# Performance work log

Hardware: AMD Instinct MI355X
Metric: run time of the kernel (lower is better)

The kernel has to match this reference:

```python
import jax, jax.numpy as jnp
import numpy as np

I, H, O = 64, 512, 64
B, S = 32, 2048


def setup_inputs() -> dict:
    key = jax.random.key(0)
    ks = jax.random.split(key, 8)
    def xavier(k, shape):
        fan_in, fan_out = shape[1], shape[0]
        lim = jnp.sqrt(6.0 / (fan_in + fan_out))
        return jax.random.uniform(k, shape, jnp.float32, -lim, lim)
    return {
        "x": jax.random.normal(ks[0], (B, S, I), jnp.float32),
        "h_0": jnp.zeros((B, H), jnp.float32),
        "Wz": xavier(ks[1], (H, I + H)),
        "Wr": xavier(ks[2], (H, I + H)),
        "Wh": xavier(ks[3], (H, I + H)),
        "bz": jnp.ones((H,), jnp.float32),
        "br": jnp.zeros((H,), jnp.float32),
        "bh": jnp.zeros((H,), jnp.float32),
        "W1": xavier(ks[4], (H, H)),
        "b1": jnp.zeros((H,), jnp.float32),
        "W2": xavier(ks[5], (O, H)),
        "b2": jnp.zeros((O,), jnp.float32),
    }


def reference(x, h_0, Wz, Wr, Wh, bz, br, bh, W1, b1, W2, b2):
    def step(h_prev, x_t):
        combined = jnp.concatenate([x_t, h_prev], axis=1)          # [B, I+H]
        z = jax.nn.sigmoid(combined @ Wz.T + bz)                   # [B, H]
        r = jax.nn.sigmoid(combined @ Wr.T + br)                   # [B, H]
        gate_input = jnp.concatenate([r * h_prev, x_t], axis=1)    # [B, H+I]
        h_hat = jnp.tanh(gate_input @ Wh.T + bh)                   # [B, H]
        h_t = (1.0 - z) * h_prev + z * h_hat
        out = jax.nn.relu(h_t @ W1.T + b1) @ W2.T + b2             # [B, O]
        return h_t, out

    # scan over time: x -> [S, B, I]
    h_last, outs = jax.lax.scan(step, h_0, jnp.swapaxes(x, 0, 1))
    return jnp.swapaxes(outs, 0, 1), h_last  # [B, S, O], [B, H]
```

## Files before the change

kernel.cpp:

```cpp
#include <hip/hip_runtime.h>
#include <stdint.h>

#define S_LEN 2048

typedef unsigned long long u64;
typedef __attribute__((ext_vector_type(8))) short short8;
typedef __attribute__((ext_vector_type(4))) float f32x4;

__device__ __forceinline__ unsigned short f2bf(float f) {
  union { float f; unsigned int u; } v; v.f = f;
  unsigned int u = v.u;
  u = (u + 0x7FFFu + ((u >> 16) & 1u)) >> 16;
  return (unsigned short)u;
}

__device__ __forceinline__ void st_bf(unsigned short* p, unsigned short v) {
  __hip_atomic_store(p, v, __ATOMIC_RELAXED, __HIP_MEMORY_SCOPE_AGENT);
}
__device__ __forceinline__ u64 ld_u64(const unsigned short* p) {
  return __hip_atomic_load((const u64*)p, __ATOMIC_RELAXED, __HIP_MEMORY_SCOPE_AGENT);
}

__global__ void prep_kernel(const float* __restrict__ Wz, const float* __restrict__ Wr,
                            const float* __restrict__ Wh, const float* __restrict__ W1,
                            const float* __restrict__ W2,
                            unsigned short* __restrict__ WgT,
                            unsigned short* __restrict__ W1T,
                            unsigned short* __restrict__ W2T) {
  const int total = 1536 * 576 + 512 * 512 + 64 * 512;
  for (int idx = blockIdx.x * 256 + threadIdx.x; idx < total; idx += gridDim.x * 256) {
    if (idx < 1536 * 576) {
      int row = idx / 576, k = idx % 576;
      float v;
      if (row < 512)       v = Wz[row * 576 + k];
      else if (row < 1024) v = Wr[(row - 512) * 576 + k];
      else {
        int r = row - 1024;
        v = (k < 64) ? Wh[r * 576 + 512 + k] : Wh[r * 576 + (k - 64)];
      }
      WgT[idx] = f2bf(v);
    } else if (idx < 1536 * 576 + 512 * 512) {
      int i = idx - 1536 * 576;
      W1T[i] = f2bf(W1[i]);
    } else {
      int i = idx - 1536 * 576 - 512 * 512;
      W2T[i] = f2bf(W2[i]);
    }
  }
}

__global__ void __launch_bounds__(256, 1) recur_kernel(
    const float* __restrict__ x, const float* __restrict__ h0,
    const float* __restrict__ bz, const float* __restrict__ br,
    const float* __restrict__ bh, const unsigned short* __restrict__ WgT,
    unsigned short* __restrict__ hbuf, unsigned short* __restrict__ rhbuf,
    unsigned short* __restrict__ h_all, float* __restrict__ h_last,
    unsigned int* __restrict__ flags) {
  extern __shared__ char smem[];
  unsigned short* Wf = (unsigned short*)smem;
  unsigned short* Xf = Wf + 6 * 18 * 64 * 8;
  float* hfp = (float*)(Xf + 2 * 64 * 8);

  const int wg = blockIdx.x;
  const int g = wg >> 4, w = wg & 15;
  const int tid = threadIdx.x;
  const int lane = tid & 63, wave = tid >> 6;
  const int crow = (lane >> 4) << 2;
  const int ccol = lane & 15;
  const int ko8 = (lane >> 4) << 3;

  for (int i = tid; i < 6 * 18 * 64; i += 256) {
    int T = i / (18 * 64);
    int kk = (i >> 6) % 18;
    int l = i & 63;
    int row = (T >> 1) * 512 + w * 32 + (T & 1) * 16 + (l & 15);
    int k = kk * 32 + ((l >> 4) << 3);
    uint4 v = *(const uint4*)(WgT + (size_t)row * 576 + k);
    *(uint4*)(Wf + (size_t)i * 8) = v;
  }
  for (int i = tid; i < 512; i += 256) {
    int m = i >> 5, c = i & 31;
    float hv = h0[(size_t)(g * 16 + m) * 512 + w * 32 + c];
    hfp[m * 32 + c] = hv;
    st_bf(hbuf + (size_t)(g * 16 + m) * 512 + w * 32 + c, f2bf(hv));
  }
  const int pm = tid >> 4, pf4 = tid & 15;
  float4 xreg = *(const float4*)(x + ((size_t)(g * 16 + pm) * S_LEN + 0) * 64 + pf4 * 4);
  {
    int c = pf4 >> 1;
    int F = (c >> 2) * 64 + (c & 3) * 16 + pm;
    unsigned short tmp[4] = {f2bf(xreg.x), f2bf(xreg.y), f2bf(xreg.z), f2bf(xreg.w)};
    *(u64*)(Xf + F * 8 + (pf4 & 1) * 4) = *(u64*)tmp;
  }
  __syncthreads();

  unsigned int* myflag = flags + g * 256 + w * 16;
  const unsigned int* gflags = flags + g * 256;
  if (tid == 0)
    __hip_atomic_store(myflag, 1u, __ATOMIC_RELAXED, __HIP_MEMORY_SCOPE_AGENT);

  float bzv = 0.f, brv = 0.f, bhv = 0.f;
  if (wave < 2) { bzv = bz[w * 32 + wave * 16 + ccol]; bhv = bh[w * 32 + wave * 16 + ccol]; }
  else          { brv = br[w * 32 + (wave & 1) * 16 + ccol]; }

  const unsigned short* hsrc  = hbuf  + (size_t)(g * 16 + ccol) * 512 + ko8;
  const unsigned short* rhsrc = rhbuf + (size_t)(g * 16 + ccol) * 512 + ko8;

  float zreg[4];

  for (int t = 0; t < S_LEN; ++t) {
    if (wave == 0) {
      const unsigned int* fl = gflags + (lane & 15) * 16;
      unsigned int it = 0;
      for (;;) {
        unsigned int v = __hip_atomic_load(fl, __ATOMIC_RELAXED, __HIP_MEMORY_SCOPE_AGENT);
        if (__all((int)(v >= (unsigned)(2 * t + 1)))) break;
        if (++it > (1u << 22)) break;
      }
    }
    __syncthreads();

    short8 aarr[16];
#pragma unroll
    for (int kk = 0; kk < 16; ++kk) {
      union { u64 q[2]; short8 v; } u;
      u.q[0] = ld_u64(hsrc + kk * 32);
      u.q[1] = ld_u64(hsrc + kk * 32 + 4);
      aarr[kk] = u.v;
    }
    const unsigned short* Bb = Wf + (size_t)wave * 18 * 512 + lane * 8;
    short8 ax0 = *(const short8*)(Xf + (0 * 64 + lane) * 8);
    short8 ax1 = *(const short8*)(Xf + (1 * 64 + lane) * 8);
    f32x4 acc0 = {0.f, 0.f, 0.f, 0.f}, acc1 = {0.f, 0.f, 0.f, 0.f};
    acc0 = __builtin_amdgcn_mfma_f32_16x16x32_bf16(ax0, *(const short8*)(Bb + 0 * 512), acc0, 0, 0, 0);
    acc1 = __builtin_amdgcn_mfma_f32_16x16x32_bf16(ax1, *(const short8*)(Bb + 1 * 512), acc1, 0, 0, 0);
#pragma unroll
    for (int kk = 0; kk < 16; kk += 2) {
      acc0 = __builtin_amdgcn_mfma_f32_16x16x32_bf16(aarr[kk],     *(const short8*)(Bb + (kk + 2) * 512), acc0, 0, 0, 0);
      acc1 = __builtin_amdgcn_mfma_f32_16x16x32_bf16(aarr[kk + 1], *(const short8*)(Bb + (kk + 3) * 512), acc1, 0, 0, 0);
    }
    f32x4 acc = acc0 + acc1;
    if (wave < 2) {
#pragma unroll
      for (int j = 0; j < 4; ++j)
        zreg[j] = 1.f / (1.f + __expf(-(acc[j] + bzv)));
    } else {
      const int nloc = (wave & 1) * 16 + ccol;
      const int ng = w * 32 + nloc;
#pragma unroll
      for (int j = 0; j < 4; ++j) {
        int m = crow + j;
        float rv = 1.f / (1.f + __expf(-(acc[j] + brv)));
        float rh = rv * hfp[m * 32 + nloc];
        st_bf(rhbuf + (size_t)(g * 16 + m) * 512 + ng, f2bf(rh));
      }
    }
    __syncthreads();
    if (tid == 0)
      __hip_atomic_store(myflag, (unsigned)(2 * t + 2), __ATOMIC_RELAXED, __HIP_MEMORY_SCOPE_AGENT);

    if (wave == 0) {
      const unsigned int* fl = gflags + (lane & 15) * 16;
      unsigned int it = 0;
      for (;;) {
        unsigned int v = __hip_atomic_load(fl, __ATOMIC_RELAXED, __HIP_MEMORY_SCOPE_AGENT);
        if (__all((int)(v >= (unsigned)(2 * t + 2)))) break;
        if (++it > (1u << 22)) break;
      }
    }
    __syncthreads();

    int tn = (t + 1 < S_LEN) ? t + 1 : t;
    xreg = *(const float4*)(x + ((size_t)(g * 16 + pm) * S_LEN + tn) * 64 + pf4 * 4);

    if (wave < 2) {
      short8 barr[16];
#pragma unroll
      for (int kk = 0; kk < 16; ++kk) {
        union { u64 q[2]; short8 v; } u2;
        u2.q[0] = ld_u64(rhsrc + kk * 32);
        u2.q[1] = ld_u64(rhsrc + kk * 32 + 4);
        barr[kk] = u2.v;
      }
      const unsigned short* Bh = Wf + (size_t)(4 + wave) * 18 * 512 + lane * 8;
      f32x4 b0 = {0.f, 0.f, 0.f, 0.f}, b1 = {0.f, 0.f, 0.f, 0.f};
      b0 = __builtin_amdgcn_mfma_f32_16x16x32_bf16(ax0, *(const short8*)(Bh + 0 * 512), b0, 0, 0, 0);
      b1 = __builtin_amdgcn_mfma_f32_16x16x32_bf16(ax1, *(const short8*)(Bh + 1 * 512), b1, 0, 0, 0);
#pragma unroll
      for (int kk = 0; kk < 16; kk += 2) {
        b0 = __builtin_amdgcn_mfma_f32_16x16x32_bf16(barr[kk],     *(const short8*)(Bh + (kk + 2) * 512), b0, 0, 0, 0);
        b1 = __builtin_amdgcn_mfma_f32_16x16x32_bf16(barr[kk + 1], *(const short8*)(Bh + (kk + 3) * 512), b1, 0, 0, 0);
      }
      f32x4 hacc = b0 + b1;
      const int nloc = wave * 16 + ccol;
      const int ng = w * 32 + nloc;
#pragma unroll
      for (int j = 0; j < 4; ++j) {
        int m = crow + j;
        float e = __expf(2.f * (hacc[j] + bhv));
        float hh = 1.f - 2.f / (e + 1.f);
        float hold = hfp[m * 32 + nloc];
        float z = zreg[j];
        float hn = (1.f - z) * hold + z * hh;
        hfp[m * 32 + nloc] = hn;
        unsigned short hb = f2bf(hn);
        st_bf(hbuf + (size_t)(g * 16 + m) * 512 + ng, hb);
        h_all[((size_t)(g * 16 + m) * S_LEN + t) * 512 + ng] = hb;
        if (t == S_LEN - 1) h_last[(size_t)(g * 16 + m) * 512 + ng] = hn;
      }
    }
    __syncthreads();
    if (tid == 0)
      __hip_atomic_store(myflag, (unsigned)(2 * t + 3), __ATOMIC_RELAXED, __HIP_MEMORY_SCOPE_AGENT);

    {
      int c = pf4 >> 1;
      int F = (c >> 2) * 64 + (c & 3) * 16 + pm;
      unsigned short tmp[4] = {f2bf(xreg.x), f2bf(xreg.y), f2bf(xreg.z), f2bf(xreg.w)};
      *(u64*)(Xf + F * 8 + (pf4 & 1) * 4) = *(u64*)tmp;
    }
  }
}

__global__ void __launch_bounds__(256, 1) head_kernel(
    const unsigned short* __restrict__ h_all, const unsigned short* __restrict__ W1T,
    const unsigned short* __restrict__ W2T, const float* __restrict__ b1,
    const float* __restrict__ b2, float* __restrict__ out) {
  extern __shared__ char smem[];
  unsigned short* hs = (unsigned short*)smem;
  unsigned short* act = hs + 64 * 520;

  const int tid = threadIdx.x, lane = tid & 63, wave = tid >> 6;
  const int crow = (lane >> 4) << 2, ccol = lane & 15;
  const size_t row0 = (size_t)blockIdx.x * 64;

  for (int i = tid; i < 64 * 64; i += 256) {
    int r = i >> 6, c8 = i & 63;
    uint4 v = *(const uint4*)(h_all + (row0 + r) * 512 + c8 * 8);
    *(uint4*)(hs + r * 520 + c8 * 8) = v;
  }
  __syncthreads();

  f32x4 acc[8][4];
#pragma unroll
  for (int nt = 0; nt < 8; ++nt)
#pragma unroll
    for (int mt = 0; mt < 4; ++mt) acc[nt][mt] = {0.f, 0.f, 0.f, 0.f};

  for (int k = 0; k < 16; ++k) {
    short8 a[4];
#pragma unroll
    for (int mt = 0; mt < 4; ++mt)
      a[mt] = *(const short8*)(hs + (mt * 16 + ccol) * 520 + k * 32 + ((lane >> 4) << 3));
#pragma unroll
    for (int nt = 0; nt < 8; ++nt) {
      int n0 = (wave * 8 + nt) * 16;
      short8 b = *(const short8*)(W1T + (size_t)(n0 + ccol) * 512 + k * 32 + ((lane >> 4) << 3));
#pragma unroll
      for (int mt = 0; mt < 4; ++mt)
        acc[nt][mt] = __builtin_amdgcn_mfma_f32_16x16x32_bf16(a[mt], b, acc[nt][mt], 0, 0, 0);
    }
  }
#pragma unroll
  for (int nt = 0; nt < 8; ++nt) {
    int n = wave * 128 + nt * 16 + ccol;
    float bias = b1[n];
#pragma unroll
    for (int mt = 0; mt < 4; ++mt)
#pragma unroll
      for (int j = 0; j < 4; ++j) {
        float v = fmaxf(acc[nt][mt][j] + bias, 0.f);
        act[(mt * 16 + crow + j) * 520 + n] = f2bf(v);
      }
  }
  __syncthreads();
  for (int i = tid; i < 64 * 64; i += 256) {
    int r = i >> 6, c8 = i & 63;
    uint4 v = *(const uint4*)(W2T + (size_t)r * 512 + c8 * 8);
    *(uint4*)(hs + r * 520 + c8 * 8) = v;
  }
  __syncthreads();

  f32x4 acc2[4];
#pragma unroll
  for (int nt = 0; nt < 4; ++nt) acc2[nt] = {0.f, 0.f, 0.f, 0.f};
  for (int k = 0; k < 16; ++k) {
    short8 a = *(const short8*)(act + (wave * 16 + ccol) * 520 + k * 32 + ((lane >> 4) << 3));
#pragma unroll
    for (int nt = 0; nt < 4; ++nt) {
      short8 b = *(const short8*)(hs + (nt * 16 + ccol) * 520 + k * 32 + ((lane >> 4) << 3));
      acc2[nt] = __builtin_amdgcn_mfma_f32_16x16x32_bf16(a, b, acc2[nt], 0, 0, 0);
    }
  }
#pragma unroll
  for (int nt = 0; nt < 4; ++nt) {
    int o = nt * 16 + ccol;
    float bias = b2[o];
#pragma unroll
    for (int j = 0; j < 4; ++j) {
      int r = wave * 16 + crow + j;
      out[(row0 + r) * 64 + o] = acc2[nt][j] + bias;
    }
  }
}

extern "C" void kernel_launch(void* const* d_in, const int* in_sizes, int n_in,
                              void* d_out, int out_size, void* d_ws, size_t ws_size,
                              hipStream_t stream) {
  const float* x  = (const float*)d_in[0];
  const float* h0 = (const float*)d_in[1];
  const float* Wz = (const float*)d_in[2];
  const float* Wr = (const float*)d_in[3];
  const float* Wh = (const float*)d_in[4];
  const float* bz = (const float*)d_in[5];
  const float* br = (const float*)d_in[6];
  const float* bh = (const float*)d_in[7];
  const float* W1 = (const float*)d_in[8];
  const float* b1 = (const float*)d_in[9];
  const float* W2 = (const float*)d_in[10];
  const float* b2 = (const float*)d_in[11];

  char* ws = (char*)d_ws;
  size_t off = 0;
  unsigned int*   flags = (unsigned int*)(ws + off);   off += 4096;
  unsigned short* hbuf  = (unsigned short*)(ws + off); off += 32 * 512 * 2;
  unsigned short* rhbuf = (unsigned short*)(ws + off); off += 32 * 512 * 2;
  unsigned short* WgT   = (unsigned short*)(ws + off); off += (size_t)1536 * 576 * 2;
  unsigned short* W1T   = (unsigned short*)(ws + off); off += (size_t)512 * 512 * 2;
  unsigned short* W2T   = (unsigned short*)(ws + off); off += (size_t)64 * 512 * 2;
  unsigned short* h_all = (unsigned short*)(ws + off); off += (size_t)32 * 2048 * 512 * 2;

  float* out = (float*)d_out;
  float* h_last = out + (size_t)32 * 2048 * 64;

  hipMemsetAsync(flags, 0, 4096, stream);
  hipLaunchKernelGGL(prep_kernel, dim3(1024), dim3(256), 0, stream,
                     Wz, Wr, Wh, W1, W2, WgT, W1T, W2T);

  const int recur_lds = (6 * 18 * 64 * 8 + 2 * 64 * 8) * 2 + 16 * 32 * 4;
  hipFuncSetAttribute(reinterpret_cast<const void*>(&recur_kernel),
                      hipFuncAttributeMaxDynamicSharedMemorySize, recur_lds);
  hipLaunchKernelGGL(recur_kernel, dim3(32), dim3(256), recur_lds, stream,
                     x, h0, bz, br, bh, WgT, hbuf, rhbuf, h_all, h_last, flags);

  const int head_lds = 2 * 64 * 520 * 2;
  hipFuncSetAttribute(reinterpret_cast<const void*>(&head_kernel),
                      hipFuncAttributeMaxDynamicSharedMemorySize, head_lds);
  hipLaunchKernelGGL(head_kernel, dim3(1024), dim3(256), head_lds, stream,
                     h_all, W1T, W2T, b1, b2, out);
}
```

Before: 17.06 ms.

## Replace flag barriers with epoch-tagged data words and double-buffered state exchange

Removes the per-step flag counters and block-wide __syncthreads barriers from the recurrent kernel. Each hidden-state and r*h value is now stored as a 32-bit word holding the bf16 value plus a timestep tag in the upper half, double-buffered by step parity. Consumers poll the data tiles directly until every tag matches, so z/h waves and r waves run as independent pipelines without a workgroup barrier. The cost is twice the exchange traffic per value and repeated polling loads of whole tiles, plus reliance on relaxed atomics for ordering. The x conversion also switches to a packed bf16 convert instruction.

```diff
diff --git a/kernel.cpp b/kernel.cpp
--- a/kernel.cpp
+++ b/kernel.cpp
@@ -4,21 +4,69 @@
 #define S_LEN 2048
 
 typedef unsigned long long u64;
+typedef unsigned int u32;
 typedef __attribute__((ext_vector_type(8))) short short8;
 typedef __attribute__((ext_vector_type(4))) float f32x4;
 
+#define XIDX(pbuf, grp, m, c) (((((pbuf)*2 + (grp))*16 + (m))*512) + (c))
+
 __device__ __forceinline__ unsigned short f2bf(float f) {
-  union { float f; unsigned int u; } v; v.f = f;
-  unsigned int u = v.u;
+  union { float f; u32 u; } v; v.f = f;
+  u32 u = v.u;
   u = (u + 0x7FFFu + ((u >> 16) & 1u)) >> 16;
   return (unsigned short)u;
 }
-
-__device__ __forceinline__ void st_bf(unsigned short* p, unsigned short v) {
+__device__ __forceinline__ float bf2f(u32 lo16) {
+  union { u32 u; float f; } v; v.u = lo16 << 16; return v.f;
+}
+__device__ __forceinline__ u32 cvt2bf(float lo, float hi) {
+  u32 r; asm("v_cvt_pk_bf16_f32 %0, %1, %2" : "=v"(r) : "v"(lo), "v"(hi)); return r;
+}
+
+__device__ __forceinline__ void st_u32(u32* p, u32 v) {
   __hip_atomic_store(p, v, __ATOMIC_RELAXED, __HIP_MEMORY_SCOPE_AGENT);
 }
-__device__ __forceinline__ u64 ld_u64(const unsigned short* p) {
-  return __hip_atomic_load((const u64*)p, __ATOMIC_RELAXED, __HIP_MEMORY_SCOPE_AGENT);
+__device__ __forceinline__ u32 ld_u32(const u32* p) {
+  return __hip_atomic_load(p, __ATOMIC_RELAXED, __HIP_MEMORY_SCOPE_AGENT);
+}
+__device__ __forceinline__ u64 ld_u64a(const u64* p) {
+  return __hip_atomic_load(p, __ATOMIC_RELAXED, __HIP_MEMORY_SCOPE_AGENT);
+}
+
+__device__ __forceinline__ bool poll_tile(const u64* base, u64 pat, u64 (&raw)[64]) {
+  u64 acc = 0;
+#pragma unroll
+  for (int kk = 0; kk < 16; ++kk)
+#pragma unroll
+    for (int q = 0; q < 4; ++q) {
+      u64 v = ld_u64a(base + kk * 16 + q);
+      raw[kk * 4 + q] = v;
+      acc |= v ^ pat;
+    }
+  return (acc & 0xFFFF0000FFFF0000ULL) == 0;
+}
+
+__device__ __forceinline__ short8 mk8(const u64* r) {
+  union { u32 w[4]; short8 v; } u;
+#pragma unroll
+  for (int q = 0; q < 4; ++q)
+    u.w[q] = (u32)(r[q] & 0xFFFFu) | (u32)((r[q] >> 16) & 0xFFFF0000u);
+  return u.v;
+}
+
+__device__ __forceinline__ f32x4 gemm18(const unsigned short* Bb, short8 xa0, short8 xa1,
+                                        const u64 (&raw)[64]) {
+  f32x4 a0 = {0.f, 0.f, 0.f, 0.f}, a1 = {0.f, 0.f, 0.f, 0.f};
+  a0 = __builtin_amdgcn_mfma_f32_16x16x32_bf16(xa0, *(const short8*)(Bb + 0 * 512), a0, 0, 0, 0);
+  a1 = __builtin_amdgcn_mfma_f32_16x16x32_bf16(xa1, *(const short8*)(Bb + 1 * 512), a1, 0, 0, 0);
+#pragma unroll
+  for (int kk = 0; kk < 16; kk += 2) {
+    a0 = __builtin_amdgcn_mfma_f32_16x16x32_bf16(mk8(&raw[kk * 4]),
+             *(const short8*)(Bb + (kk + 2) * 512), a0, 0, 0, 0);
+    a1 = __builtin_amdgcn_mfma_f32_16x16x32_bf16(mk8(&raw[(kk + 1) * 4]),
+             *(const short8*)(Bb + (kk + 3) * 512), a1, 0, 0, 0);
+  }
+  return a0 + a1;
 }
 
 __global__ void prep_kernel(const float* __restrict__ Wz, const float* __restrict__ Wr,
@@ -53,13 +101,10 @@
     const float* __restrict__ x, const float* __restrict__ h0,
     const float* __restrict__ bz, const float* __restrict__ br,
     const float* __restrict__ bh, const unsigned short* __restrict__ WgT,
-    unsigned short* __restrict__ hbuf, unsigned short* __restrict__ rhbuf,
-    unsigned short* __restrict__ h_all, float* __restrict__ h_last,
-    unsigned int* __restrict__ flags) {
+    u32* __restrict__ Hx, u32* __restrict__ RHx,
+    unsigned short* __restrict__ h_all, float* __restrict__ h_last) {
   extern __shared__ char smem[];
   unsigned short* Wf = (unsigned short*)smem;
-  unsigned short* Xf = Wf + 6 * 18 * 64 * 8;
-  float* hfp = (float*)(Xf + 2 * 64 * 8);
 
   const int wg = blockIdx.x;
   const int g = wg >> 4, w = wg & 15;
@@ -81,143 +126,123 @@
   for (int i = tid; i < 512; i += 256) {
     int m = i >> 5, c = i & 31;
     float hv = h0[(size_t)(g * 16 + m) * 512 + w * 32 + c];
-    hfp[m * 32 + c] = hv;
-    st_bf(hbuf + (size_t)(g * 16 + m) * 512 + w * 32 + c, f2bf(hv));
-  }
-  const int pm = tid >> 4, pf4 = tid & 15;
-  float4 xreg = *(const float4*)(x + ((size_t)(g * 16 + pm) * S_LEN + 0) * 64 + pf4 * 4);
-  {
-    int c = pf4 >> 1;
-    int F = (c >> 2) * 64 + (c & 3) * 16 + pm;
-    unsigned short tmp[4] = {f2bf(xreg.x), f2bf(xreg.y), f2bf(xreg.z), f2bf(xreg.w)};
-    *(u64*)(Xf + F * 8 + (pf4 & 1) * 4) = *(u64*)tmp;
+    st_u32(Hx + XIDX(0, g, m, w * 32 + c), (u32)f2bf(hv));
   }
   __syncthreads();
 
-  unsigned int* myflag = flags + g * 256 + w * 16;
-  const unsigned int* gflags = flags + g * 256;
-  if (tid == 0)
-    __hip_atomic_store(myflag, 1u, __ATOMIC_RELAXED, __HIP_MEMORY_SCOPE_AGENT);
-
-  float bzv = 0.f, brv = 0.f, bhv = 0.f;
-  if (wave < 2) { bzv = bz[w * 32 + wave * 16 + ccol]; bhv = bh[w * 32 + wave * 16 + ccol]; }
-  else          { brv = br[w * 32 + (wave & 1) * 16 + ccol]; }
-
-  const unsigned short* hsrc  = hbuf  + (size_t)(g * 16 + ccol) * 512 + ko8;
-  const unsigned short* rhsrc = rhbuf + (size_t)(g * 16 + ccol) * 512 + ko8;
-
-  float zreg[4];
-
-  for (int t = 0; t < S_LEN; ++t) {
-    if (wave == 0) {
-      const unsigned int* fl = gflags + (lane & 15) * 16;
-      unsigned int it = 0;
-      for (;;) {
-        unsigned int v = __hip_atomic_load(fl, __ATOMIC_RELAXED, __HIP_MEMORY_SCOPE_AGENT);
-        if (__all((int)(v >= (unsigned)(2 * t + 1)))) break;
-        if (++it > (1u << 22)) break;
-      }
-    }
-    __syncthreads();
-
-    short8 aarr[16];
-#pragma unroll
-    for (int kk = 0; kk < 16; ++kk) {
-      union { u64 q[2]; short8 v; } u;
-      u.q[0] = ld_u64(hsrc + kk * 32);
-      u.q[1] = ld_u64(hsrc + kk * 32 + 4);
-      aarr[kk] = u.v;
-    }
-    const unsigned short* Bb = Wf + (size_t)wave * 18 * 512 + lane * 8;
-    short8 ax0 = *(const short8*)(Xf + (0 * 64 + lane) * 8);
-    short8 ax1 = *(const short8*)(Xf + (1 * 64 + lane) * 8);
-    f32x4 acc0 = {0.f, 0.f, 0.f, 0.f}, acc1 = {0.f, 0.f, 0.f, 0.f};
-    acc0 = __builtin_amdgcn_mfma_f32_16x16x32_bf16(ax0, *(const short8*)(Bb + 0 * 512), acc0, 0, 0, 0);
-    acc1 = __builtin_amdgcn_mfma_f32_16x16x32_bf16(ax1, *(const short8*)(Bb + 1 * 512), acc1, 0, 0, 0);
-#pragma unroll
-    for (int kk = 0; kk < 16; kk += 2) {
-      acc0 = __builtin_amdgcn_mfma_f32_16x16x32_bf16(aarr[kk],     *(const short8*)(Bb + (kk + 2) * 512), acc0, 0, 0, 0);
-      acc1 = __builtin_amdgcn_mfma_f32_16x16x32_bf16(aarr[kk + 1], *(const short8*)(Bb + (kk + 3) * 512), acc1, 0, 0, 0);
-    }
-    f32x4 acc = acc0 + acc1;
-    if (wave < 2) {
+  const float* xrow = x + (size_t)(g * 16 + ccol) * (S_LEN * 64) + ko8;
+  u64 raw[64];
+
+  if (wave < 2) {
+    const int colz = w * 32 + wave * 16 + ccol;
+    const float bzv = bz[colz], bhv = bh[colz];
+    const unsigned short* Bz = Wf + (size_t)wave * 18 * 512 + lane * 8;
+    const unsigned short* Bh = Wf + (size_t)(4 + wave) * 18 * 512 + lane * 8;
+    float hold[4];
+#pragma unroll
+    for (int j = 0; j < 4; ++j)
+      hold[j] = h0[(size_t)(g * 16 + crow + j) * 512 + colz];
+
+    float4 p0 = *(const float4*)(xrow);
+    float4 p1 = *(const float4*)(xrow + 4);
+    float4 p2 = *(const float4*)(xrow + 32);
+    float4 p3 = *(const float4*)(xrow + 36);
+
+    for (int t = 0; t < S_LEN; ++t) {
+      const int pb = t & 1;
+      const u64 pat = ((u64)(u32)t << 16) | ((u64)(u32)t << 48);
+      short8 xa0, xa1;
+      {
+        union { u32 w4[4]; short8 v; } u;
+        u.w4[0] = cvt2bf(p0.x, p0.y); u.w4[1] = cvt2bf(p0.z, p0.w);
+        u.w4[2] = cvt2bf(p1.x, p1.y); u.w4[3] = cvt2bf(p1.z, p1.w);
+        xa0 = u.v;
+        u.w4[0] = cvt2bf(p2.x, p2.y); u.w4[1] = cvt2bf(p2.z, p2.w);
+        u.w4[2] = cvt2bf(p3.x, p3.y); u.w4[3] = cvt2bf(p3.z, p3.w);
+        xa1 = u.v;
+      }
+      const u64* hb = (const u64*)(Hx + XIDX(pb, g, ccol, ko8));
+      unsigned it = 0;
+      while (!__all(poll_tile(hb, pat, raw))) { if (++it > (1u << 22)) break; }
+      f32x4 zacc = gemm18(Bz, xa0, xa1, raw);
+
+      const float* xn = xrow + (size_t)((t + 1 < S_LEN) ? t + 1 : t) * 64;
+      p0 = *(const float4*)(xn);      p1 = *(const float4*)(xn + 4);
+      p2 = *(const float4*)(xn + 32); p3 = *(const float4*)(xn + 36);
+
+      float zv[4];
 #pragma unroll
       for (int j = 0; j < 4; ++j)
-        zreg[j] = 1.f / (1.f + __expf(-(acc[j] + bzv)));
-    } else {
-      const int nloc = (wave & 1) * 16 + ccol;
-      const int ng = w * 32 + nloc;
+        zv[j] = 1.f / (1.f + __expf(-(zacc[j] + bzv)));
+
+      const u64* rb = (const u64*)(RHx + XIDX(pb, g, ccol, ko8));
+      it = 0;
+      while (!__all(poll_tile(rb, pat, raw))) { if (++it > (1u << 22)) break; }
+      f32x4 hacc = gemm18(Bh, xa0, xa1, raw);
+
 #pragma unroll
       for (int j = 0; j < 4; ++j) {
-        int m = crow + j;
-        float rv = 1.f / (1.f + __expf(-(acc[j] + brv)));
-        float rh = rv * hfp[m * 32 + nloc];
-        st_bf(rhbuf + (size_t)(g * 16 + m) * 512 + ng, f2bf(rh));
-      }
-    }
-    __syncthreads();
-    if (tid == 0)
-      __hip_atomic_store(myflag, (unsigned)(2 * t + 2), __ATOMIC_RELAXED, __HIP_MEMORY_SCOPE_AGENT);
-
-    if (wave == 0) {
-      const unsigned int* fl = gflags + (lane & 15) * 16;
-      unsigned int it = 0;
-      for (;;) {
-        unsigned int v = __hip_atomic_load(fl, __ATOMIC_RELAXED, __HIP_MEMORY_SCOPE_AGENT);
-        if (__all((int)(v >= (unsigned)(2 * t + 2)))) break;
-        if (++it > (1u << 22)) break;
-      }
-    }
-    __syncthreads();
-
-    int tn = (t + 1 < S_LEN) ? t + 1 : t;
-    xreg = *(const float4*)(x + ((size_t)(g * 16 + pm) * S_LEN + tn) * 64 + pf4 * 4);
-
-    if (wave < 2) {
-      short8 barr[16];
-#pragma unroll
-      for (int kk = 0; kk < 16; ++kk) {
-        union { u64 q[2]; short8 v; } u2;
-        u2.q[0] = ld_u64(rhsrc + kk * 32);
-        u2.q[1] = ld_u64(rhsrc + kk * 32 + 4);
-        barr[kk] = u2.v;
-      }
-      const unsigned short* Bh = Wf + (size_t)(4 + wave) * 18 * 512 + lane * 8;
-      f32x4 b0 = {0.f, 0.f, 0.f, 0.f}, b1 = {0.f, 0.f, 0.f, 0.f};
-      b0 = __builtin_amdgcn_mfma_f32_16x16x32_bf16(ax0, *(const short8*)(Bh + 0 * 512), b0, 0, 0, 0);
-      b1 = __builtin_amdgcn_mfma_f32_16x16x32_bf16(ax1, *(const short8*)(Bh + 1 * 512), b1, 0, 0, 0);
-#pragma unroll
-      for (int kk = 0; kk < 16; kk += 2) {
-        b0 = __builtin_amdgcn_mfma_f32_16x16x32_bf16(barr[kk],     *(const short8*)(Bh + (kk + 2) * 512), b0, 0, 0, 0);
-        b1 = __builtin_amdgcn_mfma_f32_16x16x32_bf16(barr[kk + 1], *(const short8*)(Bh + (kk + 3) * 512), b1, 0, 0, 0);
-      }
-      f32x4 hacc = b0 + b1;
-      const int nloc = wave * 16 + ccol;
-      const int ng = w * 32 + nloc;
-#pragma unroll
-      for (int j = 0; j < 4; ++j) {
-        int m = crow + j;
         float e = __expf(2.f * (hacc[j] + bhv));
         float hh = 1.f - 2.f / (e + 1.f);
-        float hold = hfp[m * 32 + nloc];
-        float z = zreg[j];
-        float hn = (1.f - z) * hold + z * hh;
-        hfp[m * 32 + nloc] = hn;
-        unsigned short hb = f2bf(hn);
-        st_bf(hbuf + (size_t)(g * 16 + m) * 512 + ng, hb);
-        h_all[((size_t)(g * 16 + m) * S_LEN + t) * 512 + ng] = hb;
-        if (t == S_LEN - 1) h_last[(size_t)(g * 16 + m) * 512 + ng] = hn;
-      }
-    }
-    __syncthreads();
-    if (tid == 0)
-      __hip_atomic_store(myflag, (unsigned)(2 * t + 3), __ATOMIC_RELAXED, __HIP_MEMORY_SCOPE_AGENT);
-
-    {
-      int c = pf4 >> 1;
-      int F = (c >> 2) * 64 + (c & 3) * 16 + pm;
-      unsigned short tmp[4] = {f2bf(xreg.x), f2bf(xreg.y), f2bf(xreg.z), f2bf(xreg.w)};
-      *(u64*)(Xf + F * 8 + (pf4 & 1) * 4) = *(u64*)tmp;
+        float hn = (1.f - zv[j]) * hold[j] + zv[j] * hh;
+        hold[j] = hn;
+        unsigned short hbv = f2bf(hn);
+        st_u32(Hx + XIDX(pb ^ 1, g, crow + j, colz), ((u32)(t + 1) << 16) | hbv);
+        h_all[((size_t)(g * 16 + crow + j) * S_LEN + t) * 512 + colz] = hbv;
+        if (t == S_LEN - 1) h_last[(size_t)(g * 16 + crow + j) * 512 + colz] = hn;
+      }
+    }
+  } else {
+    const int nloc = (wave & 1) * 16 + ccol;
+    const int colr = w * 32 + nloc;
+    const float brv = br[colr];
+    const unsigned short* Br = Wf + (size_t)wave * 18 * 512 + lane * 8;
+
+    float4 p0 = *(const float4*)(xrow);
+    float4 p1 = *(const float4*)(xrow + 4);
+    float4 p2 = *(const float4*)(xrow + 32);
+    float4 p3 = *(const float4*)(xrow + 36);
+
+    for (int t = 0; t < S_LEN; ++t) {
+      const int pb = t & 1;
+      const u64 pat = ((u64)(u32)t << 16) | ((u64)(u32)t << 48);
+      short8 xa0, xa1;
+      {
+        union { u32 w4[4]; short8 v; } u;
+        u.w4[0] = cvt2bf(p0.x, p0.y); u.w4[1] = cvt2bf(p0.z, p0.w);
+        u.w4[2] = cvt2bf(p1.x, p1.y); u.w4[3] = cvt2bf(p1.z, p1.w);
+        xa0 = u.v;
+        u.w4[0] = cvt2bf(p2.x, p2.y); u.w4[1] = cvt2bf(p2.z, p2.w);
+        u.w4[2] = cvt2bf(p3.x, p3.y); u.w4[3] = cvt2bf(p3.z, p3.w);
+        xa1 = u.v;
+      }
+      const u64* hb = (const u64*)(Hx + XIDX(pb, g, ccol, ko8));
+      u32 hx[4];
+      unsigned it = 0;
+      for (;;) {
+        bool ok = poll_tile(hb, pat, raw);
+        u32 a32 = 0;
+#pragma unroll
+        for (int j = 0; j < 4; ++j) {
+          hx[j] = ld_u32(Hx + XIDX(pb, g, crow + j, colr));
+          a32 |= hx[j] ^ ((u32)t << 16);
+        }
+        ok = ok && ((a32 & 0xFFFF0000u) == 0);
+        if (__all(ok)) break;
+        if (++it > (1u << 22)) break;
+      }
+      f32x4 racc = gemm18(Br, xa0, xa1, raw);
+
+      const float* xn = xrow + (size_t)((t + 1 < S_LEN) ? t + 1 : t) * 64;
+      p0 = *(const float4*)(xn);      p1 = *(const float4*)(xn + 4);
+      p2 = *(const float4*)(xn + 32); p3 = *(const float4*)(xn + 36);
+
+#pragma unroll
+      for (int j = 0; j < 4; ++j) {
+        float rv = 1.f / (1.f + __expf(-(racc[j] + brv)));
+        float rh = rv * bf2f(hx[j] & 0xFFFFu);
+        st_u32(RHx + XIDX(pb, g, crow + j, colr), ((u32)t << 16) | (u32)f2bf(rh));
+      }
     }
   }
 }
@@ -322,9 +347,8 @@
 
   char* ws = (char*)d_ws;
   size_t off = 0;
-  unsigned int*   flags = (unsigned int*)(ws + off);   off += 4096;
-  unsigned short* hbuf  = (unsigned short*)(ws + off); off += 32 * 512 * 2;
-  unsigned short* rhbuf = (unsigned short*)(ws + off); off += 32 * 512 * 2;
+  u32* Hx  = (u32*)(ws + off); off += (size_t)2 * 2 * 16 * 512 * 4;
+  u32* RHx = (u32*)(ws + off); off += (size_t)2 * 2 * 16 * 512 * 4;
   unsigned short* WgT   = (unsigned short*)(ws + off); off += (size_t)1536 * 576 * 2;
   unsigned short* W1T   = (unsigned short*)(ws + off); off += (size_t)512 * 512 * 2;
   unsigned short* W2T   = (unsigned short*)(ws + off); off += (size_t)64 * 512 * 2;
@@ -333,15 +357,14 @@
   float* out = (float*)d_out;
   float* h_last = out + (size_t)32 * 2048 * 64;
 
-  hipMemsetAsync(flags, 0, 4096, stream);
   hipLaunchKernelGGL(prep_kernel, dim3(1024), dim3(256), 0, stream,
                      Wz, Wr, Wh, W1, W2, WgT, W1T, W2T);
 
-  const int recur_lds = (6 * 18 * 64 * 8 + 2 * 64 * 8) * 2 + 16 * 32 * 4;
+  const int recur_lds = 6 * 18 * 512 * 2;
   hipFuncSetAttribute(reinterpret_cast<const void*>(&recur_kernel),
                       hipFuncAttributeMaxDynamicSharedMemorySize, recur_lds);
   hipLaunchKernelGGL(recur_kernel, dim3(32), dim3(256), recur_lds, stream,
-                     x, h0, bz, br, bh, WgT, hbuf, rhbuf, h_all, h_last, flags);
+                     x, h0, bz, br, bh, WgT, Hx, RHx, h_all, h_last);
 
   const int head_lds = 2 * 64 * 520 * 2;
   hipFuncSetAttribute(reinterpret_cast<const void*>(&head_kernel),
```

New measurement: 67.82 ms. 3.98x slower.
